# Optimization experiments

Hardware: AMD Instinct MI355X
Metric: run time of the kernel (lower is better)

The kernel has to match this reference:

```python
import jax, jax.numpy as jnp
import numpy as np

D = 128  # embed dim

def linear(x, W, b):
    return x @ W.T + b

def mha1(x, w_in, b_in, w_out, b_out):
    # Single-head MultiheadAttention, x: (S, B, D), seq-first like torch.nn.MultiheadAttention
    q, k, v = jnp.split(x @ w_in.T + b_in, 3, axis=-1)
    scores = jnp.einsum('sbd,tbd->bst', q, k) / jnp.sqrt(jnp.asarray(D, x.dtype))
    att = jax.nn.softmax(scores, axis=-1)
    o = jnp.einsum('bst,tbd->sbd', att, v)
    return o @ w_out.T + b_out

def setup_inputs() -> dict:
    key = jax.random.key(0)
    ks = iter(jax.random.split(key, 32))
    def p(shape, scale=0.02):
        return (jax.random.normal(next(ks), shape, dtype=jnp.float32) * scale)
    B, S, F = 8, 2048, 3584
    inp = {
        'x': jax.random.normal(next(ks), (B, S, F), dtype=jnp.float32),
        'place_W': p((128, 2048)), 'place_b': p((128,)),
        'cast_W': p((128, 512)), 'cast_b': p((128,)),
        'action_W': p((128, 512)), 'action_b': p((128,)),
        'audio_W': p((128, 512)), 'audio_b': p((128,)),
        'e_W': p((128, 512)), 'e_b': p((128,)),
        'la_win': p((3 * D, D)), 'la_bin': p((3 * D,)),
        'la_wout': p((D, D)), 'la_bout': p((D,)),
        'be_W': p((128, 256)), 'be_b': p((128,)),
        'ba_win': p((3 * D, D)), 'ba_bin': p((3 * D,)),
        'ba_wout': p((D, D)), 'ba_bout': p((D,)),
        'bp_W': p((1, 128)), 'bp_b': p((1,)),
    }
    return inp

def reference(x, place_W, place_b, cast_W, cast_b, action_W, action_b,
              audio_W, audio_b, e_W, e_b, la_win, la_bin, la_wout, la_bout,
              be_W, be_b, ba_win, ba_bin, ba_wout, ba_bout, bp_W, bp_b):
    # --- forward_embeddings ---
    place = jax.nn.relu(linear(x[:, :, :2048], place_W, place_b))
    cast = jax.nn.relu(linear(x[:, :, 2048:2560], cast_W, cast_b))
    action = jax.nn.relu(linear(x[:, :, 2560:3072], action_W, action_b))
    audio = jax.nn.relu(linear(x[:, :, 3072:3584], audio_W, audio_b))
    feats = jnp.concatenate((place, cast, action, audio), axis=2)  # (B,S,512)
    e = jax.nn.relu(linear(feats, e_W, e_b))  # (B,S,128)
    e = jnp.transpose(e, (1, 0, 2))  # (S,B,128) seq-first
    e = mha1(e, la_win, la_bin, la_wout, la_bout)
    # --- forward_segmentation (single-pass prefix/suffix means) ---
    S = e.shape[0]
    csum = jnp.cumsum(e, axis=0)  # (S,B,D)
    total = csum[-1]
    i = jnp.arange(1, S, dtype=e.dtype)[:, None, None]
    left = csum[:-1] / i                       # mean of e[:i]
    right = (total[None] - csum[:-1]) / (S - i)  # mean of e[i:]
    cat = jnp.concatenate((left, right), axis=-1)  # (S-1,B,256)
    b = jax.nn.relu(linear(cat, be_W, be_b))
    b = mha1(b, ba_win, ba_bin, ba_wout, ba_bout)
    b = jax.nn.sigmoid(linear(b, bp_W, bp_b))[..., 0]  # (S-1,B)
    return (e, b)
```

## Files before the change

kernel.cpp:

```cpp
#include <hip/hip_runtime.h>
#include <hip/hip_bf16.h>
#include <math.h>
#include <stdint.h>


#define DEV static __device__ __forceinline__

typedef __attribute__((ext_vector_type(8))) short bf16x8;
typedef __attribute__((ext_vector_type(4))) float f32x4;

DEV uint32_t pk2bf(float a, float b) {
  __hip_bfloat162 h = __float22bfloat162_rn(make_float2(a, b));
  return *(uint32_t*)&h;
}
DEV uint2 cvt4(float4 f) {
  return make_uint2(pk2bf(f.x, f.y), pk2bf(f.z, f.w));
}
DEV uint16_t bf1(float a) { return (uint16_t)(pk2bf(a, 0.f) & 0xffffu); }
DEV float frombf(uint16_t h) {
  union { uint32_t u; float f; } v; v.u = ((uint32_t)h) << 16; return v.f;
}

#define OFF_PW      0u
#define OFF_CW      262144u
#define OFF_AW      327680u
#define OFF_UW      393216u
#define OFF_EW      458752u
#define OFF_LAWIN   524288u
#define OFF_LAWOUT  573440u
#define OFF_BEW     589824u
#define OFF_BAWIN   622592u
#define OFF_BAWOUT  671744u
#define OFF_END     688128u

struct WPtrs { const float* p[10]; };

__global__ __launch_bounds__(256) void pack_weights(WPtrs wp, uint16_t* __restrict__ WB)
{
  const uint32_t off[11] = {OFF_PW, OFF_CW, OFF_AW, OFF_UW, OFF_EW, OFF_LAWIN,
                            OFF_LAWOUT, OFF_BEW, OFF_BAWIN, OFF_BAWOUT, OFF_END};
  uint32_t h = (blockIdx.x * 256u + threadIdx.x) * 4u;
  if (h >= OFF_END) return;
  int s = 0;
  while (h >= off[s + 1]) ++s;
  float4 f = *(const float4*)(wp.p[s] + (h - off[s]));
  *(uint2*)(WB + h) = cvt4(f);
}

template<bool ABF, bool OBF, bool RELU, bool REMAP>
__global__ __launch_bounds__(256) void gemm64(
    const void* __restrict__ Ap, int lda,
    const uint16_t* __restrict__ Wb,
    const float* __restrict__ bias,
    void* __restrict__ Cp, int ldc,
    int M, int K)
{
  __shared__ __align__(16) uint16_t As[64 * 72];
  __shared__ __align__(16) uint16_t Ws[128 * 72];

  const int t  = threadIdx.x;
  const int m0 = blockIdx.x * 64;
  const int n0 = blockIdx.y * 128;
  const int w  = t >> 6, l = t & 63;
  const int ln = l & 15, qd = l >> 4;

  f32x4 acc[4][2];
#pragma unroll
  for (int i = 0; i < 4; ++i) { acc[i][0] = (f32x4){0,0,0,0}; acc[i][1] = (f32x4){0,0,0,0}; }

  const int rr = t >> 4;
  const int cl = (t & 15) * 4;
  const int r8 = t >> 3;
  const int c8 = (t & 7) * 8;

  for (int k0 = 0; k0 < K; k0 += 64) {
    __syncthreads();
    if (ABF) {
      const uint16_t* A = (const uint16_t*)Ap;
#pragma unroll
      for (int i = 0; i < 2; ++i) {
        int m = m0 + r8 + 32 * i;
        int mc = m < M ? m : M - 1;
        *(bf16x8*)(As + (size_t)(r8 + 32 * i) * 72 + c8) =
            *(const bf16x8*)(A + (size_t)mc * lda + k0 + c8);
      }
    } else {
      const float* A = (const float*)Ap;
#pragma unroll
      for (int i = 0; i < 4; ++i) {
        int m = m0 + rr + 16 * i;
        int mc = m < M ? m : M - 1;
        float4 f = *(const float4*)(A + (size_t)mc * lda + k0 + cl);
        *(uint2*)(As + (size_t)(rr + 16 * i) * 72 + cl) = cvt4(f);
      }
    }
#pragma unroll
    for (int i = 0; i < 4; ++i) {
      int n = r8 + 32 * i;
      *(bf16x8*)(Ws + (size_t)n * 72 + c8) =
          *(const bf16x8*)(Wb + (size_t)(n0 + n) * K + k0 + c8);
    }
    __syncthreads();
#pragma unroll
    for (int ks = 0; ks < 2; ++ks) {
      bf16x8 af[4], bfr[2];
#pragma unroll
      for (int mf = 0; mf < 4; ++mf)
        af[mf] = *(const bf16x8*)(As + (size_t)(mf * 16 + ln) * 72 + ks * 32 + qd * 8);
#pragma unroll
      for (int nf = 0; nf < 2; ++nf)
        bfr[nf] = *(const bf16x8*)(Ws + (size_t)(w * 32 + nf * 16 + ln) * 72 + ks * 32 + qd * 8);
#pragma unroll
      for (int mf = 0; mf < 4; ++mf)
#pragma unroll
        for (int nf = 0; nf < 2; ++nf)
          acc[mf][nf] = __builtin_amdgcn_mfma_f32_16x16x32_bf16(af[mf], bfr[nf], acc[mf][nf], 0, 0, 0);
    }
  }

#pragma unroll
  for (int mf = 0; mf < 4; ++mf) {
#pragma unroll
    for (int r = 0; r < 4; ++r) {
      int m = m0 + mf * 16 + qd * 4 + r;
      if (m < M) {
        size_t ro = REMAP ? (size_t)((m & 2047) * 8 + (m >> 11)) : (size_t)m;
#pragma unroll
        for (int nf = 0; nf < 2; ++nf) {
          int n = n0 + w * 32 + nf * 16 + ln;
          float v = acc[mf][nf][r] + bias[n];
          if (RELU) v = fmaxf(v, 0.f);
          if (OBF) ((uint16_t*)Cp)[ro * (size_t)ldc + n] = bf1(v);
          else     ((float*)Cp)[ro * (size_t)ldc + n] = v;
        }
      }
    }
  }
}

__global__ __launch_bounds__(256) void gemm_feats64(
    const float* __restrict__ x, const uint16_t* __restrict__ WB,
    const float* __restrict__ pb, const float* __restrict__ cb,
    const float* __restrict__ ab, const float* __restrict__ ub,
    uint16_t* __restrict__ feats)
{
  __shared__ __align__(16) uint16_t As[64 * 72];
  __shared__ __align__(16) uint16_t Ws[128 * 72];

  const int seg = blockIdx.y;
  const uint16_t* Wb; const float* bias; int kbase, Kseg;
  if (seg == 0)      { Wb = WB + OFF_PW; bias = pb; kbase = 0;    Kseg = 2048; }
  else if (seg == 1) { Wb = WB + OFF_CW; bias = cb; kbase = 2048; Kseg = 512; }
  else if (seg == 2) { Wb = WB + OFF_AW; bias = ab; kbase = 2560; Kseg = 512; }
  else               { Wb = WB + OFF_UW; bias = ub; kbase = 3072; Kseg = 512; }

  const int t  = threadIdx.x;
  const int m0 = blockIdx.x * 64;
  const int w  = t >> 6, l = t & 63;
  const int ln = l & 15, qd = l >> 4;

  f32x4 acc[4][2];
#pragma unroll
  for (int i = 0; i < 4; ++i) { acc[i][0] = (f32x4){0,0,0,0}; acc[i][1] = (f32x4){0,0,0,0}; }

  const int rr = t >> 4;
  const int cl = (t & 15) * 4;
  const int r8 = t >> 3;
  const int c8 = (t & 7) * 8;

  for (int k0 = 0; k0 < Kseg; k0 += 64) {
    __syncthreads();
#pragma unroll
    for (int i = 0; i < 4; ++i) {
      int m = m0 + rr + 16 * i;
      float4 f = *(const float4*)(x + (size_t)m * 3584 + kbase + k0 + cl);
      *(uint2*)(As + (size_t)(rr + 16 * i) * 72 + cl) = cvt4(f);
    }
#pragma unroll
    for (int i = 0; i < 4; ++i) {
      int n = r8 + 32 * i;
      *(bf16x8*)(Ws + (size_t)n * 72 + c8) =
          *(const bf16x8*)(Wb + (size_t)n * Kseg + k0 + c8);
    }
    __syncthreads();
#pragma unroll
    for (int ks = 0; ks < 2; ++ks) {
      bf16x8 af[4], bfr[2];
#pragma unroll
      for (int mf = 0; mf < 4; ++mf)
        af[mf] = *(const bf16x8*)(As + (size_t)(mf * 16 + ln) * 72 + ks * 32 + qd * 8);
#pragma unroll
      for (int nf = 0; nf < 2; ++nf)
        bfr[nf] = *(const bf16x8*)(Ws + (size_t)(w * 32 + nf * 16 + ln) * 72 + ks * 32 + qd * 8);
#pragma unroll
      for (int mf = 0; mf < 4; ++mf)
#pragma unroll
        for (int nf = 0; nf < 2; ++nf)
          acc[mf][nf] = __builtin_amdgcn_mfma_f32_16x16x32_bf16(af[mf], bfr[nf], acc[mf][nf], 0, 0, 0);
    }
  }

#pragma unroll
  for (int mf = 0; mf < 4; ++mf) {
#pragma unroll
    for (int r = 0; r < 4; ++r) {
      int m = m0 + mf * 16 + qd * 4 + r;
#pragma unroll
      for (int nf = 0; nf < 2; ++nf) {
        int n = w * 32 + nf * 16 + ln;
        float v = fmaxf(acc[mf][nf][r] + bias[n], 0.f);
        feats[(size_t)m * 512 + seg * 128 + n] = bf1(v);
      }
    }
  }
}

__global__ __launch_bounds__(256) void gemm_becat64(
    const float* __restrict__ csum, const float* __restrict__ part,
    const uint16_t* __restrict__ Wb, const float* __restrict__ bias,
    uint16_t* __restrict__ C)
{
  __shared__ __align__(16) uint16_t As[64 * 72];
  __shared__ __align__(16) uint16_t Ws[128 * 72];

  const int M = 16376, K = 256;
  const int t  = threadIdx.x;
  const int m0 = blockIdx.x * 64;
  const int w  = t >> 6, l = t & 63;
  const int ln = l & 15, qd = l >> 4;

  f32x4 acc[4][2];
#pragma unroll
  for (int i = 0; i < 4; ++i) { acc[i][0] = (f32x4){0,0,0,0}; acc[i][1] = (f32x4){0,0,0,0}; }

  const int rr = t >> 4;
  const int cl = (t & 15) * 4;
  const int r8 = t >> 3;
  const int c8 = (t & 7) * 8;

  for (int k0 = 0; k0 < K; k0 += 64) {
    __syncthreads();
#pragma unroll
    for (int i = 0; i < 4; ++i) {
      int m = m0 + rr + 16 * i;
      int mc = m < M ? m : M - 1;
      int j = mc >> 3, bb = mc & 7;
      int kk = k0 + cl;
      float4 f;
      if (kk < 128) {
        float4 v = *(const float4*)(csum + (size_t)mc * 128 + kk);
        float4 p = *(const float4*)(part + (size_t)(bb * 64 + (j >> 5)) * 128 + kk);
        float s = 1.f / (float)(j + 1);
        f = make_float4((v.x + p.x) * s, (v.y + p.y) * s,
                        (v.z + p.z) * s, (v.w + p.w) * s);
      } else {
        int d = kk - 128;
        float4 c0 = *(const float4*)(csum + (size_t)mc * 128 + d);
        float4 p0 = *(const float4*)(part + (size_t)(bb * 64 + (j >> 5)) * 128 + d);
        float4 ct = *(const float4*)(csum + (size_t)(16376 + bb) * 128 + d);
        float4 pt = *(const float4*)(part + (size_t)(bb * 64 + 63) * 128 + d);
        float s = 1.f / (float)(2047 - j);
        f = make_float4(((ct.x + pt.x) - (c0.x + p0.x)) * s,
                        ((ct.y + pt.y) - (c0.y + p0.y)) * s,
                        ((ct.z + pt.z) - (c0.z + p0.z)) * s,
                        ((ct.w + pt.w) - (c0.w + p0.w)) * s);
      }
      *(uint2*)(As + (size_t)(rr + 16 * i) * 72 + cl) = cvt4(f);
    }
#pragma unroll
    for (int i = 0; i < 4; ++i) {
      int n = r8 + 32 * i;
      *(bf16x8*)(Ws + (size_t)n * 72 + c8) =
          *(const bf16x8*)(Wb + (size_t)n * K + k0 + c8);
    }
    __syncthreads();
#pragma unroll
    for (int ks = 0; ks < 2; ++ks) {
      bf16x8 af[4], bfr[2];
#pragma unroll
      for (int mf = 0; mf < 4; ++mf)
        af[mf] = *(const bf16x8*)(As + (size_t)(mf * 16 + ln) * 72 + ks * 32 + qd * 8);
#pragma unroll
      for (int nf = 0; nf < 2; ++nf)
        bfr[nf] = *(const bf16x8*)(Ws + (size_t)(w * 32 + nf * 16 + ln) * 72 + ks * 32 + qd * 8);
#pragma unroll
      for (int mf = 0; mf < 4; ++mf)
#pragma unroll
        for (int nf = 0; nf < 2; ++nf)
          acc[mf][nf] = __builtin_amdgcn_mfma_f32_16x16x32_bf16(af[mf], bfr[nf], acc[mf][nf], 0, 0, 0);
    }
  }

#pragma unroll
  for (int mf = 0; mf < 4; ++mf) {
#pragma unroll
    for (int r = 0; r < 4; ++r) {
      int m = m0 + mf * 16 + qd * 4 + r;
      if (m < M) {
#pragma unroll
        for (int nf = 0; nf < 2; ++nf) {
          int n = w * 32 + nf * 16 + ln;
          C[(size_t)m * 128 + n] = bf1(fmaxf(acc[mf][nf][r] + bias[n], 0.f));
        }
      }
    }
  }
}

__global__ __launch_bounds__(256) void vpack(
    const uint16_t* __restrict__ proj, uint16_t* __restrict__ Vtb, int Slen)
{
  __shared__ __align__(16) uint16_t Vs[64][136];

  const int kt = blockIdx.x, b = blockIdx.y, t = threadIdx.x;
  const int sl = t >> 2, cg = (t & 3) * 32;
  const int s  = kt * 64 + sl;
  const int valid = s < Slen;
  const int sc2 = valid ? s : Slen - 1;
  const uint16_t* src = proj + ((size_t)sc2 * 8 + b) * 384 + 256 + cg;
#pragma unroll
  for (int i = 0; i < 4; ++i) {
    bf16x8 v;
    if (valid) v = *(const bf16x8*)(src + i * 8);
    else       v = (bf16x8){0,0,0,0,0,0,0,0};
    *(bf16x8*)(&Vs[sl][cg + i * 8]) = v;
  }
  __syncthreads();
  const int d = t >> 1, hh = t & 1;
  uint32_t wv[16];
#pragma unroll
  for (int i = 0; i < 16; ++i) {
    int K = 32 * hh + 16 * ((i >> 1) & 1) + 4 * ((i >> 2) & 3) + 2 * (i & 1);
    wv[i] = (uint32_t)Vs[K][d] | ((uint32_t)Vs[K + 1][d] << 16);
  }
  uint16_t* dv = Vtb + (((size_t)b * 32 + kt) * 128 + d) * 64 + hh * 32;
#pragma unroll
  for (int i = 0; i < 4; ++i)
    *(uint4*)(dv + i * 8) = *(uint4*)(&wv[i * 4]);
}

__global__ __launch_bounds__(256, 3) void attn_split3(
    const uint16_t* __restrict__ proj, const uint16_t* __restrict__ Vtb,
    float* __restrict__ Opart, float* __restrict__ ml, int Slen)
{
  __shared__ __align__(16) uint16_t KsL[64 * 136];
  __shared__ __align__(16) uint16_t VtL[128 * 72];

  const int t  = threadIdx.x;
  const int b  = blockIdx.y;
  const int q0 = blockIdx.x * 64;
  const int split = blockIdx.z;
  const int kbeg = split * 704;
  const int kend = (split == 2) ? Slen : kbeg + 704;
  const int w  = t >> 6;
  const int l  = t & 63;
  const int ln = l & 15;
  const int qd = l >> 4;
  const float scl = 0.08838834764831845f;

  const int kkey = t >> 2, kcg = (t & 3) * 32;
  const int vd   = t >> 1, vh  = (t & 1) * 32;

  bf16x8 qf[4];
  {
    int qrow = q0 + w * 16 + ln;
    int qc = qrow < Slen ? qrow : Slen - 1;
    const uint16_t* qp = proj + ((size_t)qc * 8 + b) * 384 + qd * 8;
#pragma unroll
    for (int ks = 0; ks < 4; ++ks) {
      union { bf16x8 v; uint16_t h[8]; uint32_t u[4]; } in, out;
      in.v = *(const bf16x8*)(qp + ks * 32);
#pragma unroll
      for (int j = 0; j < 4; ++j)
        out.u[j] = pk2bf(frombf(in.h[2 * j]) * scl, frombf(in.h[2 * j + 1]) * scl);
      qf[ks] = out.v;
    }
  }

  f32x4 oacc[8];
#pragma unroll
  for (int i = 0; i < 8; ++i) oacc[i] = (f32x4){0.f, 0.f, 0.f, 0.f};
  float mrow = -INFINITY;
  float lrow = 0.f;

  const int ntiles = (kend - kbeg + 63) >> 6;

  bf16x8 kreg[4], vreg[4];
  {
    int kg = kbeg + kkey;
    int kc = kg < Slen ? kg : Slen - 1;
    const uint16_t* ksrc = proj + ((size_t)kc * 8 + b) * 384 + 128 + kcg;
#pragma unroll
    for (int i = 0; i < 4; ++i) kreg[i] = *(const bf16x8*)(ksrc + i * 8);
    const uint16_t* vsrc = Vtb + (((size_t)b * 32 + 11 * split) * 128 + vd) * 64 + vh;
#pragma unroll
    for (int i = 0; i < 4; ++i) vreg[i] = *(const bf16x8*)(vsrc + i * 8);
  }

  for (int kt = 0; kt < ntiles; ++kt) {
    __syncthreads();
    {
      uint16_t* kdst = KsL + kkey * 136 + kcg;
#pragma unroll
      for (int i = 0; i < 4; ++i) *(bf16x8*)(kdst + i * 8) = kreg[i];
      uint16_t* vdst = VtL + vd * 72 + vh;
#pragma unroll
      for (int i = 0; i < 4; ++i) *(bf16x8*)(vdst + i * 8) = vreg[i];
    }
    if (kt + 1 < ntiles) {
      int kg = kbeg + (kt + 1) * 64 + kkey;
      int kc = kg < Slen ? kg : Slen - 1;
      const uint16_t* ksrc = proj + ((size_t)kc * 8 + b) * 384 + 128 + kcg;
#pragma unroll
      for (int i = 0; i < 4; ++i) kreg[i] = *(const bf16x8*)(ksrc + i * 8);
      const int tile = 11 * split + kt + 1;
      const uint16_t* vsrc = Vtb + (((size_t)b * 32 + tile) * 128 + vd) * 64 + vh;
#pragma unroll
      for (int i = 0; i < 4; ++i) vreg[i] = *(const bf16x8*)(vsrc + i * 8);
    }
    __syncthreads();

    float sc[4][4];
#pragma unroll
    for (int nf = 0; nf < 4; ++nf) {
      f32x4 acc = (f32x4){0.f, 0.f, 0.f, 0.f};
#pragma unroll
      for (int ks = 0; ks < 4; ++ks) {
        bf16x8 kf = *(const bf16x8*)(KsL + (size_t)(nf * 16 + ln) * 136 + ks * 32 + qd * 8);
        acc = __builtin_amdgcn_mfma_f32_16x16x32_bf16(kf, qf[ks], acc, 0, 0, 0);
      }
      int keyb = kbeg + kt * 64 + nf * 16 + qd * 4;
#pragma unroll
      for (int r = 0; r < 4; ++r)
        sc[nf][r] = (keyb + r < kend) ? acc[r] : -1e30f;
    }

    float mx = sc[0][0];
#pragma unroll
    for (int nf = 0; nf < 4; ++nf)
#pragma unroll
      for (int r = 0; r < 4; ++r) mx = fmaxf(mx, sc[nf][r]);
    mx = fmaxf(mx, __shfl_xor(mx, 16));
    mx = fmaxf(mx, __shfl_xor(mx, 32));
    float mNew = fmaxf(mrow, mx);

    float ps = 0.f;
#pragma unroll
    for (int nf = 0; nf < 4; ++nf) {
      float p0 = __expf(sc[nf][0] - mNew);
      float p1 = __expf(sc[nf][1] - mNew);
      float p2 = __expf(sc[nf][2] - mNew);
      float p3 = __expf(sc[nf][3] - mNew);
      sc[nf][0] = p0; sc[nf][1] = p1; sc[nf][2] = p2; sc[nf][3] = p3;
      ps += (p0 + p1) + (p2 + p3);
    }
    ps += __shfl_xor(ps, 16);
    ps += __shfl_xor(ps, 32);

    float alpha = __expf(mrow - mNew);
    mrow = mNew;
    lrow = lrow * alpha + ps;

    float alphaR[4];
#pragma unroll
    for (int r = 0; r < 4; ++r)
      alphaR[r] = __shfl(alpha, (l & 48) | (qd * 4 + r));
#pragma unroll
    for (int no = 0; no < 8; ++no) {
#pragma unroll
      for (int r = 0; r < 4; ++r) oacc[no][r] *= alphaR[r];
    }

    union { bf16x8 v; uint32_t u[4]; } pa0, pa1;
#pragma unroll
    for (int i = 0; i < 4; ++i) {
      pa0.u[i] = pk2bf(sc[(i >> 1)][(i & 1) * 2],     sc[(i >> 1)][(i & 1) * 2 + 1]);
      pa1.u[i] = pk2bf(sc[2 + (i >> 1)][(i & 1) * 2], sc[2 + (i >> 1)][(i & 1) * 2 + 1]);
    }
#pragma unroll
    for (int no = 0; no < 8; ++no) {
      bf16x8 vf = *(const bf16x8*)(VtL + (size_t)(no * 16 + ln) * 72 + qd * 8);
      oacc[no] = __builtin_amdgcn_mfma_f32_16x16x32_bf16(pa0.v, vf, oacc[no], 0, 0, 0);
    }
#pragma unroll
    for (int no = 0; no < 8; ++no) {
      bf16x8 vf = *(const bf16x8*)(VtL + (size_t)(no * 16 + ln) * 72 + 32 + qd * 8);
      oacc[no] = __builtin_amdgcn_mfma_f32_16x16x32_bf16(pa1.v, vf, oacc[no], 0, 0, 0);
    }
  }

#pragma unroll
  for (int r = 0; r < 4; ++r) {
    int qg = q0 + w * 16 + qd * 4 + r;
    if (qg < Slen) {
      size_t row = (size_t)qg * 8 + b;
      float* dst = Opart + ((size_t)split * 16384 + row) * 128 + ln;
#pragma unroll
      for (int no = 0; no < 8; ++no) dst[no * 16] = oacc[no][r];
    }
  }
  {
    int qg = q0 + w * 16 + ln;
    if (qd == 0 && qg < Slen) {
      size_t row = (size_t)qg * 8 + b;
      ml[((size_t)split * 16384 + row) * 2 + 0] = mrow;
      ml[((size_t)split * 16384 + row) * 2 + 1] = lrow;
    }
  }
}

template<bool HEAD>
__global__ __launch_bounds__(256) void gemm_attc64(
    const float* __restrict__ Opart, const float* __restrict__ ml,
    const uint16_t* __restrict__ Wb,
    const float* __restrict__ bias,
    const float* __restrict__ bpW, const float* __restrict__ bpb,
    float* __restrict__ out, int M)
{
  __shared__ __align__(16) uint16_t As[64 * 72];
  __shared__ __align__(16) uint16_t Ws[128 * 72];
  __shared__ float RW[64][4];
  __shared__ float Ct[HEAD ? 64 : 1][133];

  const int K = 128;
  const int t  = threadIdx.x;
  const int m0 = blockIdx.x * 64;
  const int w  = t >> 6, l = t & 63;
  const int ln = l & 15, qd = l >> 4;

  if (t < 64) {
    int m = m0 + t;
    int mc = m < M ? m : M - 1;
    float m0v = ml[(size_t)mc * 2],                 l0 = ml[(size_t)mc * 2 + 1];
    float m1v = ml[((size_t)16384 + mc) * 2],       l1 = ml[((size_t)16384 + mc) * 2 + 1];
    float m2v = ml[((size_t)32768 + mc) * 2],       l2 = ml[((size_t)32768 + mc) * 2 + 1];
    float Mx = fmaxf(fmaxf(m0v, m1v), m2v);
    float w0 = __expf(m0v - Mx), w1 = __expf(m1v - Mx), w2 = __expf(m2v - Mx);
    RW[t][0] = w0; RW[t][1] = w1; RW[t][2] = w2;
    RW[t][3] = 1.f / (l0 * w0 + l1 * w1 + l2 * w2);
  }

  f32x4 acc[4][2];
#pragma unroll
  for (int i = 0; i < 4; ++i) { acc[i][0] = (f32x4){0,0,0,0}; acc[i][1] = (f32x4){0,0,0,0}; }

  const int rr = t >> 4;
  const int cl = (t & 15) * 4;
  const int r8 = t >> 3;
  const int c8 = (t & 7) * 8;

  for (int k0 = 0; k0 < K; k0 += 64) {
    __syncthreads();
#pragma unroll
    for (int i = 0; i < 4; ++i) {
      int m = m0 + rr + 16 * i;
      int mc = m < M ? m : M - 1;
      int kk = k0 + cl;
      float4 a = *(const float4*)(Opart + (size_t)mc * 128 + kk);
      float4 c = *(const float4*)(Opart + ((size_t)16384 + mc) * 128 + kk);
      float4 e = *(const float4*)(Opart + ((size_t)32768 + mc) * 128 + kk);
      int rl = rr + 16 * i;
      float w0 = RW[rl][0], w1 = RW[rl][1], w2 = RW[rl][2], inv = RW[rl][3];
      float4 f = make_float4((a.x * w0 + c.x * w1 + e.x * w2) * inv,
                             (a.y * w0 + c.y * w1 + e.y * w2) * inv,
                             (a.z * w0 + c.z * w1 + e.z * w2) * inv,
                             (a.w * w0 + c.w * w1 + e.w * w2) * inv);
      *(uint2*)(As + (size_t)rl * 72 + cl) = cvt4(f);
    }
#pragma unroll
    for (int i = 0; i < 4; ++i) {
      int n = r8 + 32 * i;
      *(bf16x8*)(Ws + (size_t)n * 72 + c8) =
          *(const bf16x8*)(Wb + (size_t)n * K + k0 + c8);
    }
    __syncthreads();
#pragma unroll
    for (int ks = 0; ks < 2; ++ks) {
      bf16x8 af[4], bfr[2];
#pragma unroll
      for (int mf = 0; mf < 4; ++mf)
        af[mf] = *(const bf16x8*)(As + (size_t)(mf * 16 + ln) * 72 + ks * 32 + qd * 8);
#pragma unroll
      for (int nf = 0; nf < 2; ++nf)
        bfr[nf] = *(const bf16x8*)(Ws + (size_t)(w * 32 + nf * 16 + ln) * 72 + ks * 32 + qd * 8);
#pragma unroll
      for (int mf = 0; mf < 4; ++mf)
#pragma unroll
        for (int nf = 0; nf < 2; ++nf)
          acc[mf][nf] = __builtin_amdgcn_mfma_f32_16x16x32_bf16(af[mf], bfr[nf], acc[mf][nf], 0, 0, 0);
    }
  }

  if (HEAD) {
    __syncthreads();
#pragma unroll
    for (int mf = 0; mf < 4; ++mf) {
#pragma unroll
      for (int r = 0; r < 4; ++r) {
        int rowL = mf * 16 + qd * 4 + r;
#pragma unroll
        for (int nf = 0; nf < 2; ++nf) {
          int n = w * 32 + nf * 16 + ln;
          Ct[rowL][n] = acc[mf][nf][r] + bias[n];
        }
      }
    }
    __syncthreads();
    int row = t >> 2, qg = t & 3;
    int m = m0 + row;
    float p = 0.f;
#pragma unroll
    for (int j = 0; j < 32; ++j) {
      int c = qg + j * 4;
      p += Ct[row][c] * bpW[c];
    }
    p += __shfl_xor(p, 1);
    p += __shfl_xor(p, 2);
    if (qg == 0 && m < M)
      out[m] = 1.f / (1.f + __expf(-(p + bpb[0])));
  } else {
#pragma unroll
    for (int mf = 0; mf < 4; ++mf) {
#pragma unroll
      for (int r = 0; r < 4; ++r) {
        int m = m0 + mf * 16 + qd * 4 + r;
        if (m < M) {
#pragma unroll
          for (int nf = 0; nf < 2; ++nf) {
            int n = w * 32 + nf * 16 + ln;
            out[(size_t)m * 128 + n] = acc[mf][nf][r] + bias[n];
          }
        }
      }
    }
  }
}

__global__ void cumsum_p1(const float* __restrict__ e, float* __restrict__ csum,
                          float* __restrict__ part)
{
  int chunk = blockIdx.x, b = blockIdx.y, d = threadIdx.x;
  float run = 0.f;
  int s0 = chunk * 32;
  for (int s = 0; s < 32; ++s) {
    size_t idx = ((size_t)(s0 + s) * 8 + b) * 128 + d;
    run += e[idx];
    csum[idx] = run;
  }
  part[(b * 64 + chunk) * 128 + d] = run;
}

__global__ void cumsum_p2(float* __restrict__ part)
{
  int b = blockIdx.x, d = threadIdx.x;
  float run = 0.f;
  for (int c = 0; c < 64; ++c) {
    float v = part[(b * 64 + c) * 128 + d];
    part[(b * 64 + c) * 128 + d] = run;
    run += v;
  }
}

extern "C" void kernel_launch(void* const* d_in, const int* in_sizes, int n_in,
                              void* d_out, int out_size, void* d_ws, size_t ws_size,
                              hipStream_t stream)
{
  const float* x       = (const float*)d_in[0];
  const float* pW      = (const float*)d_in[1];
  const float* pb      = (const float*)d_in[2];
  const float* cW      = (const float*)d_in[3];
  const float* cb      = (const float*)d_in[4];
  const float* aW      = (const float*)d_in[5];
  const float* ab      = (const float*)d_in[6];
  const float* uW      = (const float*)d_in[7];
  const float* ub      = (const float*)d_in[8];
  const float* eW      = (const float*)d_in[9];
  const float* eb      = (const float*)d_in[10];
  const float* la_win  = (const float*)d_in[11];
  const float* la_bin  = (const float*)d_in[12];
  const float* la_wout = (const float*)d_in[13];
  const float* la_bout = (const float*)d_in[14];
  const float* beW     = (const float*)d_in[15];
  const float* beb     = (const float*)d_in[16];
  const float* ba_win  = (const float*)d_in[17];
  const float* ba_bin  = (const float*)d_in[18];
  const float* ba_wout = (const float*)d_in[19];
  const float* ba_bout = (const float*)d_in[20];
  const float* bpW     = (const float*)d_in[21];
  const float* bpb     = (const float*)d_in[22];

  float* ws   = (float*)d_ws;
  float* outF = (float*)d_out;

  uint16_t* WB  = (uint16_t*)ws;
  float* base   = ws + 344064;
  uint16_t* featsB = (uint16_t*)base;
  float* csumB  = base;
  float* partB  = base + 2097152;
  uint16_t* eB  = (uint16_t*)(base + 4194304);
  uint16_t* projB = (uint16_t*)(base + 5242880);
  uint16_t* VtbB  = (uint16_t*)(base + 8388608);
  float* OpartB = base + 9437184;
  float* mlB    = base + 15728640;

  WPtrs wp;
  wp.p[0] = pW; wp.p[1] = cW; wp.p[2] = aW; wp.p[3] = uW; wp.p[4] = eW;
  wp.p[5] = la_win; wp.p[6] = la_wout; wp.p[7] = beW; wp.p[8] = ba_win; wp.p[9] = ba_wout;
  pack_weights<<<dim3(672), 256, 0, stream>>>(wp, WB);

  gemm_feats64<<<dim3(256, 4), 256, 0, stream>>>(x, WB, pb, cb, ab, ub, featsB);
  gemm64<true, true, true, true><<<dim3(256, 1), 256, 0, stream>>>(
      featsB, 512, WB + OFF_EW, eb, eB, 128, 16384, 512);
  gemm64<true, true, false, false><<<dim3(256, 3), 256, 0, stream>>>(
      eB, 128, WB + OFF_LAWIN, la_bin, projB, 384, 16384, 128);
  vpack<<<dim3(32, 8), 256, 0, stream>>>(projB, VtbB, 2048);
  attn_split3<<<dim3(32, 8, 3), 256, 0, stream>>>(projB, VtbB, OpartB, mlB, 2048);
  gemm_attc64<false><<<dim3(256), 256, 0, stream>>>(
      OpartB, mlB, WB + OFF_LAWOUT, la_bout, nullptr, nullptr, outF, 16384);
  cumsum_p1<<<dim3(64, 8), 128, 0, stream>>>(outF, csumB, partB);
  cumsum_p2<<<dim3(8), 128, 0, stream>>>(partB);
  gemm_becat64<<<dim3(256), 256, 0, stream>>>(csumB, partB, WB + OFF_BEW, beb, eB);
  gemm64<true, true, false, false><<<dim3(256, 3), 256, 0, stream>>>(
      eB, 128, WB + OFF_BAWIN, ba_bin, projB, 384, 16376, 128);
  vpack<<<dim3(32, 8), 256, 0, stream>>>(projB, VtbB, 2047);
  attn_split3<<<dim3(32, 8, 3), 256, 0, stream>>>(projB, VtbB, OpartB, mlB, 2047);
  gemm_attc64<true><<<dim3(256), 256, 0, stream>>>(
      OpartB, mlB, WB + OFF_BAWOUT, ba_bout, bpW, bpb, outF + 2097152, 16376);
}
```

Baseline: 519.3 us.

## Register-prefetch next K tile in GEMMs and attention, replace syncthreads with raw barriers

Restructures the GEMM, segment-embedding, attention and combine-output kernels so global loads for the next K tile go into registers while MFMAs run on the current LDS tile. This hides global memory latency behind compute. __syncthreads is replaced by explicit waitcnt plus raw s_barrier, and s_setprio is raised around the MFMA sections in the attention kernel. Register pressure goes up, which could lower occupancy, and the hand-written waits add ordering risk.

```diff
diff --git a/kernel.cpp b/kernel.cpp
--- a/kernel.cpp
+++ b/kernel.cpp
@@ -20,6 +20,10 @@
 DEV float frombf(uint16_t h) {
   union { uint32_t u; float f; } v; v.u = ((uint32_t)h) << 16; return v.f;
 }
+
+#define WAIT_VM0()  __asm__ volatile("s_waitcnt vmcnt(0)" ::: "memory")
+#define WAIT_LGKM0() __asm__ volatile("s_waitcnt lgkmcnt(0)" ::: "memory")
+#define RAW_BARRIER() __builtin_amdgcn_s_barrier()
 
 #define OFF_PW      0u
 #define OFF_CW      262144u
@@ -73,16 +77,18 @@
   const int r8 = t >> 3;
   const int c8 = (t & 7) * 8;
 
-  for (int k0 = 0; k0 < K; k0 += 64) {
-    __syncthreads();
+  float4 a32[4];
+  bf16x8 a16[2];
+  bf16x8 wreg[4];
+
+  auto loadA = [&](int k0) {
     if (ABF) {
       const uint16_t* A = (const uint16_t*)Ap;
 #pragma unroll
       for (int i = 0; i < 2; ++i) {
         int m = m0 + r8 + 32 * i;
         int mc = m < M ? m : M - 1;
-        *(bf16x8*)(As + (size_t)(r8 + 32 * i) * 72 + c8) =
-            *(const bf16x8*)(A + (size_t)mc * lda + k0 + c8);
+        a16[i] = *(const bf16x8*)(A + (size_t)mc * lda + k0 + c8);
       }
     } else {
       const float* A = (const float*)Ap;
@@ -90,17 +96,37 @@
       for (int i = 0; i < 4; ++i) {
         int m = m0 + rr + 16 * i;
         int mc = m < M ? m : M - 1;
-        float4 f = *(const float4*)(A + (size_t)mc * lda + k0 + cl);
-        *(uint2*)(As + (size_t)(rr + 16 * i) * 72 + cl) = cvt4(f);
+        a32[i] = *(const float4*)(A + (size_t)mc * lda + k0 + cl);
       }
     }
 #pragma unroll
     for (int i = 0; i < 4; ++i) {
       int n = r8 + 32 * i;
-      *(bf16x8*)(Ws + (size_t)n * 72 + c8) =
-          *(const bf16x8*)(Wb + (size_t)(n0 + n) * K + k0 + c8);
-    }
-    __syncthreads();
+      wreg[i] = *(const bf16x8*)(Wb + (size_t)(n0 + n) * K + k0 + c8);
+    }
+  };
+  auto writeLDS = [&]() {
+    if (ABF) {
+#pragma unroll
+      for (int i = 0; i < 2; ++i)
+        *(bf16x8*)(As + (size_t)(r8 + 32 * i) * 72 + c8) = a16[i];
+    } else {
+#pragma unroll
+      for (int i = 0; i < 4; ++i)
+        *(uint2*)(As + (size_t)(rr + 16 * i) * 72 + cl) = cvt4(a32[i]);
+    }
+#pragma unroll
+    for (int i = 0; i < 4; ++i)
+      *(bf16x8*)(Ws + (size_t)(r8 + 32 * i) * 72 + c8) = wreg[i];
+  };
+
+  loadA(0);
+  for (int k0 = 0; k0 < K; k0 += 64) {
+    WAIT_VM0();
+    writeLDS();
+    WAIT_LGKM0();
+    RAW_BARRIER();
+    if (k0 + 64 < K) loadA(k0 + 64);
 #pragma unroll
     for (int ks = 0; ks < 2; ++ks) {
       bf16x8 af[4], bfr[2];
@@ -116,6 +142,7 @@
         for (int nf = 0; nf < 2; ++nf)
           acc[mf][nf] = __builtin_amdgcn_mfma_f32_16x16x32_bf16(af[mf], bfr[nf], acc[mf][nf], 0, 0, 0);
     }
+    RAW_BARRIER();
   }
 
 #pragma unroll
@@ -168,21 +195,34 @@
   const int r8 = t >> 3;
   const int c8 = (t & 7) * 8;
 
+  float4 a32[4];
+  bf16x8 wreg[4];
+
+  auto loadA = [&](int k0) {
+#pragma unroll
+    for (int i = 0; i < 4; ++i) {
+      int m = m0 + rr + 16 * i;
+      a32[i] = *(const float4*)(x + (size_t)m * 3584 + kbase + k0 + cl);
+    }
+#pragma unroll
+    for (int i = 0; i < 4; ++i) {
+      int n = r8 + 32 * i;
+      wreg[i] = *(const bf16x8*)(Wb + (size_t)n * Kseg + k0 + c8);
+    }
+  };
+
+  loadA(0);
   for (int k0 = 0; k0 < Kseg; k0 += 64) {
-    __syncthreads();
-#pragma unroll
-    for (int i = 0; i < 4; ++i) {
-      int m = m0 + rr + 16 * i;
-      float4 f = *(const float4*)(x + (size_t)m * 3584 + kbase + k0 + cl);
-      *(uint2*)(As + (size_t)(rr + 16 * i) * 72 + cl) = cvt4(f);
-    }
-#pragma unroll
-    for (int i = 0; i < 4; ++i) {
-      int n = r8 + 32 * i;
-      *(bf16x8*)(Ws + (size_t)n * 72 + c8) =
-          *(const bf16x8*)(Wb + (size_t)n * Kseg + k0 + c8);
-    }
-    __syncthreads();
+    WAIT_VM0();
+#pragma unroll
+    for (int i = 0; i < 4; ++i)
+      *(uint2*)(As + (size_t)(rr + 16 * i) * 72 + cl) = cvt4(a32[i]);
+#pragma unroll
+    for (int i = 0; i < 4; ++i)
+      *(bf16x8*)(Ws + (size_t)(r8 + 32 * i) * 72 + c8) = wreg[i];
+    WAIT_LGKM0();
+    RAW_BARRIER();
+    if (k0 + 64 < Kseg) loadA(k0 + 64);
 #pragma unroll
     for (int ks = 0; ks < 2; ++ks) {
       bf16x8 af[4], bfr[2];
@@ -198,6 +238,7 @@
         for (int nf = 0; nf < 2; ++nf)
           acc[mf][nf] = __builtin_amdgcn_mfma_f32_16x16x32_bf16(af[mf], bfr[nf], acc[mf][nf], 0, 0, 0);
     }
+    RAW_BARRIER();
   }
 
 #pragma unroll
@@ -386,19 +427,21 @@
   const int ntiles = (kend - kbeg + 63) >> 6;
 
   bf16x8 kreg[4], vreg[4];
-  {
-    int kg = kbeg + kkey;
+  auto loadTile = [&](int kt) {
+    int kg = kbeg + kt * 64 + kkey;
     int kc = kg < Slen ? kg : Slen - 1;
     const uint16_t* ksrc = proj + ((size_t)kc * 8 + b) * 384 + 128 + kcg;
 #pragma unroll
     for (int i = 0; i < 4; ++i) kreg[i] = *(const bf16x8*)(ksrc + i * 8);
-    const uint16_t* vsrc = Vtb + (((size_t)b * 32 + 11 * split) * 128 + vd) * 64 + vh;
+    const int tile = 11 * split + kt;
+    const uint16_t* vsrc = Vtb + (((size_t)b * 32 + tile) * 128 + vd) * 64 + vh;
 #pragma unroll
     for (int i = 0; i < 4; ++i) vreg[i] = *(const bf16x8*)(vsrc + i * 8);
-  }
-
+  };
+
+  loadTile(0);
   for (int kt = 0; kt < ntiles; ++kt) {
-    __syncthreads();
+    WAIT_VM0();
     {
       uint16_t* kdst = KsL + kkey * 136 + kcg;
 #pragma unroll
@@ -407,20 +450,12 @@
 #pragma unroll
       for (int i = 0; i < 4; ++i) *(bf16x8*)(vdst + i * 8) = vreg[i];
     }
-    if (kt + 1 < ntiles) {
-      int kg = kbeg + (kt + 1) * 64 + kkey;
-      int kc = kg < Slen ? kg : Slen - 1;
-      const uint16_t* ksrc = proj + ((size_t)kc * 8 + b) * 384 + 128 + kcg;
-#pragma unroll
-      for (int i = 0; i < 4; ++i) kreg[i] = *(const bf16x8*)(ksrc + i * 8);
-      const int tile = 11 * split + kt + 1;
-      const uint16_t* vsrc = Vtb + (((size_t)b * 32 + tile) * 128 + vd) * 64 + vh;
-#pragma unroll
-      for (int i = 0; i < 4; ++i) vreg[i] = *(const bf16x8*)(vsrc + i * 8);
-    }
-    __syncthreads();
+    WAIT_LGKM0();
+    RAW_BARRIER();
+    if (kt + 1 < ntiles) loadTile(kt + 1);
 
     float sc[4][4];
+    __builtin_amdgcn_s_setprio(1);
 #pragma unroll
     for (int nf = 0; nf < 4; ++nf) {
       f32x4 acc = (f32x4){0.f, 0.f, 0.f, 0.f};
@@ -434,6 +469,7 @@
       for (int r = 0; r < 4; ++r)
         sc[nf][r] = (keyb + r < kend) ? acc[r] : -1e30f;
     }
+    __builtin_amdgcn_s_setprio(0);
 
     float mx = sc[0][0];
 #pragma unroll
@@ -477,6 +513,7 @@
       pa0.u[i] = pk2bf(sc[(i >> 1)][(i & 1) * 2],     sc[(i >> 1)][(i & 1) * 2 + 1]);
       pa1.u[i] = pk2bf(sc[2 + (i >> 1)][(i & 1) * 2], sc[2 + (i >> 1)][(i & 1) * 2 + 1]);
     }
+    __builtin_amdgcn_s_setprio(1);
 #pragma unroll
     for (int no = 0; no < 8; ++no) {
       bf16x8 vf = *(const bf16x8*)(VtL + (size_t)(no * 16 + ln) * 72 + qd * 8);
@@ -487,6 +524,8 @@
       bf16x8 vf = *(const bf16x8*)(VtL + (size_t)(no * 16 + ln) * 72 + 32 + qd * 8);
       oacc[no] = __builtin_amdgcn_mfma_f32_16x16x32_bf16(pa1.v, vf, oacc[no], 0, 0, 0);
     }
+    __builtin_amdgcn_s_setprio(0);
+    RAW_BARRIER();
   }
 
 #pragma unroll
@@ -539,6 +578,7 @@
     RW[t][0] = w0; RW[t][1] = w1; RW[t][2] = w2;
     RW[t][3] = 1.f / (l0 * w0 + l1 * w1 + l2 * w2);
   }
+  __syncthreads();
 
   f32x4 acc[4][2];
 #pragma unroll
@@ -549,31 +589,45 @@
   const int r8 = t >> 3;
   const int c8 = (t & 7) * 8;
 
-  for (int k0 = 0; k0 < K; k0 += 64) {
-    __syncthreads();
+  float4 ra[4], rc[4], re[4];
+  bf16x8 wreg[4];
+
+  auto loadA = [&](int k0) {
 #pragma unroll
     for (int i = 0; i < 4; ++i) {
       int m = m0 + rr + 16 * i;
       int mc = m < M ? m : M - 1;
       int kk = k0 + cl;
-      float4 a = *(const float4*)(Opart + (size_t)mc * 128 + kk);
-      float4 c = *(const float4*)(Opart + ((size_t)16384 + mc) * 128 + kk);
-      float4 e = *(const float4*)(Opart + ((size_t)32768 + mc) * 128 + kk);
+      ra[i] = *(const float4*)(Opart + (size_t)mc * 128 + kk);
+      rc[i] = *(const float4*)(Opart + ((size_t)16384 + mc) * 128 + kk);
+      re[i] = *(const float4*)(Opart + ((size_t)32768 + mc) * 128 + kk);
+    }
+#pragma unroll
+    for (int i = 0; i < 4; ++i) {
+      int n = r8 + 32 * i;
+      wreg[i] = *(const bf16x8*)(Wb + (size_t)n * K + k0 + c8);
+    }
+  };
+
+  loadA(0);
+  for (int k0 = 0; k0 < K; k0 += 64) {
+    WAIT_VM0();
+#pragma unroll
+    for (int i = 0; i < 4; ++i) {
       int rl = rr + 16 * i;
       float w0 = RW[rl][0], w1 = RW[rl][1], w2 = RW[rl][2], inv = RW[rl][3];
-      float4 f = make_float4((a.x * w0 + c.x * w1 + e.x * w2) * inv,
-                             (a.y * w0 + c.y * w1 + e.y * w2) * inv,
-                             (a.z * w0 + c.z * w1 + e.z * w2) * inv,
-                             (a.w * w0 + c.w * w1 + e.w * w2) * inv);
+      float4 f = make_float4((ra[i].x * w0 + rc[i].x * w1 + re[i].x * w2) * inv,
+                             (ra[i].y * w0 + rc[i].y * w1 + re[i].y * w2) * inv,
+                             (ra[i].z * w0 + rc[i].z * w1 + re[i].z * w2) * inv,
+                             (ra[i].w * w0 + rc[i].w * w1 + re[i].w * w2) * inv);
       *(uint2*)(As + (size_t)rl * 72 + cl) = cvt4(f);
     }
 #pragma unroll
-    for (int i = 0; i < 4; ++i) {
-      int n = r8 + 32 * i;
-      *(bf16x8*)(Ws + (size_t)n * 72 + c8) =
-          *(const bf16x8*)(Wb + (size_t)n * K + k0 + c8);
-    }
-    __syncthreads();
+    for (int i = 0; i < 4; ++i)
+      *(bf16x8*)(Ws + (size_t)(r8 + 32 * i) * 72 + c8) = wreg[i];
+    WAIT_LGKM0();
+    RAW_BARRIER();
+    if (k0 + 64 < K) loadA(k0 + 64);
 #pragma unroll
     for (int ks = 0; ks < 2; ++ks) {
       bf16x8 af[4], bfr[2];
@@ -589,6 +643,7 @@
         for (int nf = 0; nf < 2; ++nf)
           acc[mf][nf] = __builtin_amdgcn_mfma_f32_16x16x32_bf16(af[mf], bfr[nf], acc[mf][nf], 0, 0, 0);
     }
+    RAW_BARRIER();
   }
 
   if (HEAD) {
```

Measured after the change: 517.1 us. Within noise of the previous version (-0.4%).
